# Kernel optimization log

Hardware: AMD Instinct MI355X
Metric: run time of the kernel (lower is better)

The kernel has to match this reference:

```python
import jax, jax.numpy as jnp
import numpy as np

D_MODEL = 1024
SCALE = 1.0 / np.sqrt(D_MODEL).astype(np.float32)


def setup_inputs() -> dict:
    key = jax.random.key(0)
    ks = jax.random.split(key, 9)
    B, S, D = 4, 2048, D_MODEL
    init = 1.0 / np.sqrt(D).astype(np.float32)
    return {
        "q": jax.random.normal(ks[0], (B, S, D), jnp.float32),
        "k": jax.random.normal(ks[1], (B, S, D), jnp.float32),
        "v": jax.random.normal(ks[2], (B, S, D), jnp.float32),
        "Wq": jax.random.uniform(ks[3], (D, D), jnp.float32, -init, init),
        "bq": jax.random.uniform(ks[4], (D,), jnp.float32, -init, init),
        "Wk": jax.random.uniform(ks[5], (D, D), jnp.float32, -init, init),
        "bk": jax.random.uniform(ks[6], (D,), jnp.float32, -init, init),
        "Wv": jax.random.uniform(ks[7], (D, D), jnp.float32, -init, init),
        "bv": jax.random.uniform(ks[8], (D,), jnp.float32, -init, init),
    }


def reference(q, k, v, Wq, bq, Wk, bk, Wv, bv):
    # Linear projections (torch Linear: x @ W.T + b)
    qp = jnp.einsum('bsd,ed->bse', q, Wq) + bq
    kp = jnp.einsum('bsd,ed->bse', k, Wk) + bk
    vp = jnp.einsum('bsd,ed->bse', v, Wv) + bv
    qp = jax.nn.softmax(qp, axis=-1)          # softmax over feature dim
    kp = jax.nn.softmax(kp, axis=-2) * SCALE  # softmax over sequence dim
    vp = jax.nn.softmax(vp, axis=-2)          # softmax over sequence dim
    attn_weights = jnp.einsum('bqd,bkd->bqk', qp, kp)  # [B,S,S]
    output = jnp.einsum('bqk,bkd->bqd', attn_weights, vp)
    return (output, attn_weights)
```

## Files before the change

### kernel.cpp

```cpp
#include <hip/hip_runtime.h>
#include <math.h>


typedef float  f32x4  __attribute__((ext_vector_type(4)));
typedef __bf16 bf16x8 __attribute__((ext_vector_type(8)));
typedef int    i32x4  __attribute__((ext_vector_type(4)));
typedef unsigned short u16;

__device__ __forceinline__ float b2f(u16 u) {
    unsigned int i = ((unsigned int)u) << 16; float f;
    __builtin_memcpy(&f, &i, 4); return f;
}
__device__ __forceinline__ u16 f2b(float f) {
    unsigned int i; __builtin_memcpy(&i, &f, 4);
    i += 0x7FFFu + ((i >> 16) & 1u);
    return (u16)(i >> 16);
}

__global__ __launch_bounds__(256) void cvt_all(
    const float4* __restrict__ q, const float4* __restrict__ k,
    const float4* __restrict__ v, const float4* __restrict__ Wq,
    const float4* __restrict__ Wk, const float4* __restrict__ Wv,
    const float* __restrict__ bq, const float* __restrict__ bk,
    const float* __restrict__ bv,
    ushort4* __restrict__ qb, ushort4* __restrict__ kb,
    ushort4* __restrict__ vb, ushort4* __restrict__ Wb,
    float* __restrict__ biasCat)
{
    int bid = blockIdx.x, t = threadIdx.x;
    const float4* s; ushort4* d; int idx;
    if (bid < 8192)       { s = q;  d = qb;            idx = bid * 256 + t; }
    else if (bid < 16384) { s = k;  d = kb;            idx = (bid - 8192) * 256 + t; }
    else if (bid < 24576) { s = v;  d = vb;            idx = (bid - 16384) * 256 + t; }
    else if (bid < 25600) { s = Wq; d = Wb;            idx = (bid - 24576) * 256 + t; }
    else if (bid < 26624) { s = Wk; d = Wb + 262144;   idx = (bid - 25600) * 256 + t; }
    else if (bid < 27648) { s = Wv; d = Wb + 524288;   idx = (bid - 26624) * 256 + t; }
    else {
        for (int i = t; i < 3072; i += 256)
            biasCat[i] = (i < 1024) ? bq[i] : (i < 2048) ? bk[i - 1024] : bv[i - 2048];
        return;
    }
    float4 vv = s[idx];
    ushort4 o;
    o.x = f2b(vv.x); o.y = f2b(vv.y); o.z = f2b(vv.z); o.w = f2b(vv.w);
    d[idx] = o;
}

__global__ __launch_bounds__(512, 2) void gemm256_attn(
    const u16* __restrict__ Ap, const u16* __restrict__ Bp,
    float* __restrict__ C32, u16* __restrict__ C16,
    int N, int K, long long sA, long long sB, long long sC)
{
    __shared__ __align__(16) u16 lds[65536];

    const int tid  = threadIdx.x;
    const int lane = tid & 63;
    const int w    = tid >> 6;
    const int wr   = w >> 2, wc = w & 3;

    const int gx  = gridDim.x;
    const int tot = gx * gridDim.y;
    const int lin = blockIdx.y * gx + blockIdx.x;
    const int vlin = (lin & 7) * (tot >> 3) + (lin >> 3);
    const int bx = vlin % gx, by = vlin / gx;
    const int m0 = by * 256, n0 = bx * 256;
    const int z  = blockIdx.z;

    const u16* Ag = Ap + (size_t)z * sA;
    const u16* Bg = Bp + (size_t)z * sB;

    const int cl = tid ^ ((tid >> 4) & 6);
    const int lr = cl >> 3;
    const int ce = (cl & 7) * 8;
    const int arow = m0 + lr;
    const int brow = n0 + (lr & 31) + ((lr & 32) << 1);

    const int axr = ((lane >> 2) & 3) << 4;
    const int ar0 = (wr * 64 + (lane & 15)) * 64 + (lane >> 4) * 8;
    const int br0 = (wc * 32 + (lane & 15)) * 64 + (lane >> 4) * 8;

#define GLL16(gsrc, ldsoff)                                                    \
    __builtin_amdgcn_global_load_lds(                                          \
        (__attribute__((address_space(1))) void*)(uintptr_t)(gsrc),            \
        (__attribute__((address_space(3))) void*)&lds[ldsoff], 16, 0, 0)

#define STAGE_A(c, h, T)                                                       \
    do { const u16* _s = Ag + (size_t)(arow + (h) * 64) * K + (T) * 64 + ce;   \
         int _d = (((c) << 1) + (h)) * 8192 + tid * 8;                         \
         GLL16(_s, _d); GLL16(_s + (size_t)128 * K, _d + 4096); } while (0)

#define STAGE_B(c, g, T)                                                       \
    do { const u16* _s = Bg + (size_t)(brow + (g) * 32) * K + (T) * 64 + ce;   \
         int _d = 32768 + (((c) << 1) + (g)) * 8192 + tid * 8;                 \
         GLL16(_s, _d); GLL16(_s + (size_t)128 * K, _d + 4096); } while (0)

#define SBAR asm volatile("s_barrier" ::: "memory")
#define LGKM0 do { asm volatile("s_waitcnt lgkmcnt(0)" ::: "memory");          \
                   __builtin_amdgcn_sched_barrier(0); } while (0)

#define LDA(base)                                                              \
    _Pragma("unroll") for (int mi2 = 0; mi2 < 4; ++mi2)                        \
    _Pragma("unroll") for (int ks = 0; ks < 2; ++ks)                           \
        afr[mi2][ks] = __builtin_bit_cast(bf16x8,                              \
            *(const i32x4*)&lds[(base) + ((ar0 + mi2 * 1024 + ks * 32) ^ axr)]);

#define LDB(dst, base)                                                         \
    _Pragma("unroll") for (int ni2 = 0; ni2 < 2; ++ni2)                        \
    _Pragma("unroll") for (int ks = 0; ks < 2; ++ks)                           \
        dst[ni2][ks] = __builtin_bit_cast(bf16x8,                              \
            *(const i32x4*)&lds[(base) + ((br0 + ni2 * 1024 + ks * 32) ^ axr)]);

#define MFMA_Q(mb, nb, bfrag)                                                  \
    __builtin_amdgcn_s_setprio(1);                                             \
    _Pragma("unroll") for (int mi2 = 0; mi2 < 4; ++mi2)                        \
    _Pragma("unroll") for (int ni2 = 0; ni2 < 2; ++ni2)                        \
    _Pragma("unroll") for (int ks = 0; ks < 2; ++ks)                           \
        acc[(mb) + mi2][(nb) + ni2] = __builtin_amdgcn_mfma_f32_16x16x32_bf16( \
            afr[mi2][ks], bfrag[ni2][ks], acc[(mb) + mi2][(nb) + ni2], 0, 0, 0); \
    __builtin_amdgcn_s_setprio(0)

    f32x4 acc[8][4];
#pragma unroll
    for (int i = 0; i < 8; ++i)
#pragma unroll
        for (int j = 0; j < 4; ++j) acc[i][j] = (f32x4)0.0f;

    bf16x8 afr[4][2], b0f[2][2], b1f[2][2];

    const int nt = K >> 6;

    STAGE_A(0, 0, 0); STAGE_B(0, 0, 0);
    STAGE_A(0, 1, 0); STAGE_B(0, 1, 0);
    STAGE_A(1, 0, 1); STAGE_B(1, 0, 1);

    for (int T = 0; T < nt; ++T) {
        const int cur = T & 1, nxt = cur ^ 1;
        const int ab = (cur << 1) * 8192;
        const int bb = 32768 + (cur << 1) * 8192;

        if (T + 1 < nt) asm volatile("s_waitcnt vmcnt(4)" ::: "memory");
        else            asm volatile("s_waitcnt vmcnt(0)" ::: "memory");
        SBAR;
        LDA(ab); LDB(b0f, bb);
        if (T + 1 < nt) STAGE_B(nxt, 1, T + 1);
        SBAR; LGKM0;
        MFMA_Q(0, 0, b0f);
        SBAR;
        LDB(b1f, bb + 8192);
        if (T + 1 < nt) STAGE_A(nxt, 1, T + 1);
        SBAR; LGKM0;
        MFMA_Q(0, 2, b1f);
        SBAR;
        LDA(ab + 8192);
        if (T + 2 < nt) STAGE_A(cur, 0, T + 2);
        SBAR; LGKM0;
        MFMA_Q(4, 0, b0f);
        SBAR;
        if (T + 2 < nt) STAGE_B(cur, 0, T + 2);
        SBAR; LGKM0;
        MFMA_Q(4, 2, b1f);
        SBAR;
    }

    const int cr0 = m0 + wr * 128 + ((lane >> 4) << 2);
    const int cc0 = n0 + wc * 64 + (lane & 15);
    float* Cg = C32 + (size_t)z * sC;
#pragma unroll
    for (int mi = 0; mi < 8; ++mi)
#pragma unroll
        for (int ni = 0; ni < 4; ++ni)
#pragma unroll
            for (int j = 0; j < 4; ++j)
                Cg[(size_t)(cr0 + mi * 16 + j) * N + cc0 + ni * 16] = acc[mi][ni][j];

    u16* sE = lds;
    u16* Cb = C16 + (size_t)z * sC;
    const int wrow0 = ((lane >> 4) << 2);
    const int wcol0 = wc * 64 + (lane & 15);
    const int rr = tid >> 2;
    const int c0 = (tid & 3) * 8;
    __syncthreads();
#pragma unroll
    for (int p = 0; p < 2; ++p) {
        if (wr == p) {
#pragma unroll
            for (int mi = 0; mi < 8; ++mi)
#pragma unroll
                for (int ni = 0; ni < 4; ++ni)
#pragma unroll
                    for (int j = 0; j < 4; ++j)
                        sE[(wrow0 + mi * 16 + j) * 264 + wcol0 + ni * 16] =
                            f2b(acc[mi][ni][j]);
        }
        __syncthreads();
#pragma unroll
        for (int i = 0; i < 8; ++i) {
            i32x4 vv = *(const i32x4*)&sE[rr * 264 + c0 + i * 32];
            *(i32x4*)&Cb[(size_t)(m0 + p * 128 + rr) * N + n0 + c0 + i * 32] = vv;
        }
        if (p == 0) __syncthreads();
    }
#undef GLL16
#undef STAGE_A
#undef STAGE_B
#undef LDA
#undef LDB
#undef MFMA_Q
}

template<int EPI, int BM>
__global__ __launch_bounds__(256, 2) void gemm_bw(
    const u16* __restrict__ Ap, const u16* __restrict__ Bp,
    float* __restrict__ C32, u16* __restrict__ C16, u16* __restrict__ Calt,
    const float* __restrict__ bias,
    int N, int K, long long sA, long long sB, long long sC)
{
    constexpr int AMI = BM / 32;
    constexpr int ALD = BM / 64;
    constexpr int ASZ = BM * 32;
    constexpr int BUF = ASZ + 4096;
    __shared__ __align__(16) u16 lds[3 * BUF];

    const int tid  = threadIdx.x;
    const int lane = tid & 63;
    const int w    = tid >> 6;
    const int wr   = w >> 1, wc = w & 1;

    const int gx  = gridDim.x;
    const int tot = gx * gridDim.y;
    const int lin = blockIdx.y * gx + blockIdx.x;
    const int vlin = (lin & 7) * (tot >> 3) + (lin >> 3);
    const int bx = vlin % gx, by = vlin / gx;
    const int m0 = by * BM, n0 = bx * 128;
    const int z  = blockIdx.z;

    const u16* Ag = Ap + (size_t)z * sA;
    const u16* Bg = Bp + (size_t)z * sB;

    const int cltid = tid ^ ((tid >> 3) & 3);
    const int crow  = cltid >> 2;
    const int ce    = (cltid & 3) * 8;

    const int exr = ((lane >> 1) & 3) << 3;
    const int ar0 = (wr * (BM / 2) + (lane & 15)) * 32 + (lane >> 4) * 8;
    const int br0 = (wc * 64 + (lane & 15)) * 32 + (lane >> 4) * 8;

#define GLLW(gsrc, ldsoff)                                                     \
    __builtin_amdgcn_global_load_lds(                                          \
        (__attribute__((address_space(1))) void*)(uintptr_t)(gsrc),            \
        (__attribute__((address_space(3))) void*)&lds[ldsoff], 16, 0, 0)

#define STAGE(buf, T)                                                          \
    do {                                                                       \
        _Pragma("unroll") for (int ld = 0; ld < ALD; ++ld)                     \
            GLLW(Ag + (size_t)(m0 + ld * 64 + crow) * K + (T) * 32 + ce,       \
                 (buf) + ld * 2048 + tid * 8);                                 \
        _Pragma("unroll") for (int ld = 0; ld < 2; ++ld)                       \
            GLLW(Bg + (size_t)(n0 + ld * 64 + crow) * K + (T) * 32 + ce,       \
                 (buf) + ASZ + ld * 2048 + tid * 8);                           \
    } while (0)

#define LGKM0B do { asm volatile("s_waitcnt lgkmcnt(0)" ::: "memory");         \
                    __builtin_amdgcn_sched_barrier(0); } while (0)

    f32x4 acc[AMI][4];
#pragma unroll
    for (int i = 0; i < AMI; ++i)
#pragma unroll
        for (int j = 0; j < 4; ++j) acc[i][j] = (f32x4)0.0f;

    bf16x8 afr[AMI], bfr[4];

    const int nt = K >> 5;

    int b0 = 0, b1 = BUF, b2 = 2 * BUF;
    STAGE(b0, 0); STAGE(b1, 1);

    for (int T = 0; T < nt; ++T) {
        if (T + 1 < nt) {
            if constexpr (BM == 256) asm volatile("s_waitcnt vmcnt(6)" ::: "memory");
            else                     asm volatile("s_waitcnt vmcnt(4)" ::: "memory");
        } else {
            asm volatile("s_waitcnt vmcnt(0)" ::: "memory");
        }
        asm volatile("s_barrier" ::: "memory");
#pragma unroll
        for (int mi = 0; mi < AMI; ++mi)
            afr[mi] = __builtin_bit_cast(bf16x8,
                *(const i32x4*)&lds[b0 + ((ar0 + mi * 512) ^ exr)]);
#pragma unroll
        for (int ni = 0; ni < 4; ++ni)
            bfr[ni] = __builtin_bit_cast(bf16x8,
                *(const i32x4*)&lds[b0 + ASZ + ((br0 + ni * 512) ^ exr)]);
        if (T + 2 < nt) STAGE(b2, T + 2);
        LGKM0B;
        __builtin_amdgcn_s_setprio(1);
#pragma unroll
        for (int mi = 0; mi < AMI; ++mi)
#pragma unroll
            for (int ni = 0; ni < 4; ++ni)
                acc[mi][ni] = __builtin_amdgcn_mfma_f32_16x16x32_bf16(
                    afr[mi], bfr[ni], acc[mi][ni], 0, 0, 0);
        __builtin_amdgcn_s_setprio(0);
        int tmp = b0; b0 = b1; b1 = b2; b2 = tmp;
    }

    if constexpr (EPI == 1) {
        u16* sE = lds;
        u16* Cb = (z == 2) ? Calt : (C16 + (size_t)z * sC);
        const int colb = wc * 64 + (lane & 15);
        float bv[4];
#pragma unroll
        for (int ni = 0; ni < 4; ++ni)
            bv[ni] = bias[(size_t)z * 1024 + n0 + colb + ni * 16];
        const int wrow0 = wr * (BM / 2) + ((lane >> 4) << 2);
        __syncthreads();
#pragma unroll
        for (int mi = 0; mi < AMI; ++mi)
#pragma unroll
            for (int ni = 0; ni < 4; ++ni)
#pragma unroll
                for (int j = 0; j < 4; ++j)
                    sE[(wrow0 + mi * 16 + j) * 136 + colb + ni * 16] =
                        f2b(__expf(acc[mi][ni][j] + bv[ni]));
        __syncthreads();
        const int rr = tid >> 2, c0 = (tid & 3) * 8;
#pragma unroll
        for (int rb = 0; rb < BM / 64; ++rb) {
            int row = rb * 64 + rr;
#pragma unroll
            for (int i = 0; i < 4; ++i) {
                i32x4 vv = *(const i32x4*)&sE[row * 136 + c0 + i * 32];
                *(i32x4*)&Cb[(size_t)(m0 + row) * N + n0 + c0 + i * 32] = vv;
            }
        }
    } else {
        float* Cg = C32 + (size_t)z * sC;
        const int cr0 = m0 + wr * (BM / 2) + ((lane >> 4) << 2);
        const int cc0 = n0 + wc * 64 + (lane & 15);
#pragma unroll
        for (int mi = 0; mi < AMI; ++mi)
#pragma unroll
            for (int ni = 0; ni < 4; ++ni)
#pragma unroll
                for (int j = 0; j < 4; ++j)
                    Cg[(size_t)(cr0 + mi * 16 + j) * N + cc0 + ni * 16] =
                        acc[mi][ni][j];
    }
#undef GLLW
#undef STAGE
#undef LGKM0B
}

__global__ __launch_bounds__(256) void sm_partials(
    u16* __restrict__ qE, const u16* __restrict__ kE, const u16* __restrict__ vE,
    float* __restrict__ kpart, float* __restrict__ vpart)
{
    int bid = blockIdx.x, t = threadIdx.x;
    if (bid < 8192) {
        u16* p = qE + (size_t)bid * 1024;
        ushort4 v = *(ushort4*)&p[t * 4];
        float e0 = b2f(v.x), e1 = b2f(v.y), e2 = b2f(v.z), e3 = b2f(v.w);
        float s = (e0 + e1) + (e2 + e3);
#pragma unroll
        for (int off = 32; off; off >>= 1) s += __shfl_down(s, off);
        __shared__ float red[4];
        if ((t & 63) == 0) red[t >> 6] = s;
        __syncthreads();
        float inv = 1.0f / ((red[0] + red[1]) + (red[2] + red[3]));
        ushort4 o;
        o.x = f2b(e0 * inv); o.y = f2b(e1 * inv);
        o.z = f2b(e2 * inv); o.w = f2b(e3 * inv);
        *(ushort4*)&p[t * 4] = o;
    } else {
        int j = bid - 8192;
        const u16* d; float* part;
        if (j < 64) { d = kE; part = kpart; } else { d = vE; part = vpart; j -= 64; }
        int b = j >> 4, c = j & 15;
        const u16* base = d + ((size_t)b * 2048 + c * 128) * 1024 + t * 4;
        float a0 = 0, a1 = 0, a2 = 0, a3 = 0;
        for (int s = 0; s < 128; ++s) {
            ushort4 v = *(const ushort4*)(base + (size_t)s * 1024);
            a0 += b2f(v.x); a1 += b2f(v.y); a2 += b2f(v.z); a3 += b2f(v.w);
        }
        *(float4*)(part + ((size_t)(b * 16 + c)) * 1024 + t * 4) = make_float4(a0, a1, a2, a3);
    }
}

__global__ __launch_bounds__(256) void col_reduce2(
    const float* __restrict__ kpart, const float* __restrict__ vpart,
    float* __restrict__ kinv, float* __restrict__ vinv)
{
    int bid = blockIdx.x;
    const float* part; float* inv; float mult;
    if (bid < 16) { part = kpart; inv = kinv; mult = 0.03125f; }
    else          { part = vpart; inv = vinv; mult = 1.0f; bid -= 16; }
    int idx = bid * 256 + threadIdx.x;
    int b = idx >> 10, e = idx & 1023;
    float s = 0;
    for (int c = 0; c < 16; ++c) s += part[((size_t)(b * 16 + c)) * 1024 + e];
    inv[idx] = mult / s;
}

__global__ __launch_bounds__(256) void norm_all(
    u16* __restrict__ kE, const float* __restrict__ kinv,
    const u16* __restrict__ vE, const float* __restrict__ vinv,
    u16* __restrict__ vpT)
{
    int bid = blockIdx.x, t = threadIdx.x;
    if (bid < 8192) {
        int b = bid >> 11, s = bid & 2047;
        u16* p = kE + ((size_t)b * 2048 + s) * 1024 + t * 4;
        float4 iv = *(const float4*)(kinv + b * 1024 + t * 4);
        ushort4 v = *(ushort4*)p;
        v.x = f2b(b2f(v.x) * iv.x); v.y = f2b(b2f(v.y) * iv.y);
        v.z = f2b(b2f(v.z) * iv.z); v.w = f2b(b2f(v.w) * iv.w);
        *(ushort4*)p = v;
    } else {
        __shared__ __align__(16) u16 tile[64][68];
        int j = bid - 8192;
        int b = j >> 9, y = (j >> 5) & 15, x = j & 31;
        int s0 = x * 64, e0 = y * 64;
        int lr = t >> 4, lc = (t & 15) * 4;
#pragma unroll
        for (int i = 0; i < 4; ++i) {
            int sr = i * 16 + lr;
            ushort4 v = *(const ushort4*)(vE + ((size_t)b * 2048 + s0 + sr) * 1024 + e0 + lc);
            tile[sr][lc] = v.x; tile[sr][lc + 1] = v.y;
            tile[sr][lc + 2] = v.z; tile[sr][lc + 3] = v.w;
        }
        __syncthreads();
#pragma unroll
        for (int i = 0; i < 4; ++i) {
            int er = i * 16 + lr;
            float iv = vinv[b * 1024 + e0 + er];
            ushort4 v;
            v.x = f2b(b2f(tile[lc + 0][er]) * iv);
            v.y = f2b(b2f(tile[lc + 1][er]) * iv);
            v.z = f2b(b2f(tile[lc + 2][er]) * iv);
            v.w = f2b(b2f(tile[lc + 3][er]) * iv);
            *(ushort4*)(vpT + ((size_t)b * 1024 + e0 + er) * 2048 + s0 + lc) = v;
        }
    }
}

extern "C" void kernel_launch(void* const* d_in, const int* in_sizes, int n_in,
                              void* d_out, int out_size, void* d_ws, size_t ws_size,
                              hipStream_t stream)
{
    const float* q  = (const float*)d_in[0];
    const float* k  = (const float*)d_in[1];
    const float* v  = (const float*)d_in[2];
    const float* Wq = (const float*)d_in[3];
    const float* bq = (const float*)d_in[4];
    const float* Wk = (const float*)d_in[5];
    const float* bk = (const float*)d_in[6];
    const float* Wv = (const float*)d_in[7];
    const float* bv = (const float*)d_in[8];

    float* out  = (float*)d_out;
    float* attn = out + 8388608;

    u16* wsU = (u16*)d_ws;
    u16* qE   = wsU;
    u16* kE   = wsU + 8388608;
    u16* Wb   = wsU + 16777216;
    u16* qb   = wsU + 25165824;
    u16* kb   = wsU + 33554432;
    u16* vb   = wsU + 41943040;
    u16* vpT  = wsU + 25165824;
    u16* attnB = wsU + 33554432;
    u16* vE   = (u16*)attn;

    float* tail  = (float*)(wsU + 50331648);
    float* kpart = tail;
    float* vpart = tail + 65536;
    float* kinv  = tail + 131072;
    float* vinv  = tail + 135168;
    float* biasCat = tail + 139264;

    const long long SD = 2048LL * 1024, SS = 2048LL * 2048, DS = 1024LL * 2048;

    cvt_all<<<dim3(27649), dim3(256), 0, stream>>>(
        (const float4*)q, (const float4*)k, (const float4*)v,
        (const float4*)Wq, (const float4*)Wk, (const float4*)Wv,
        bq, bk, bv,
        (ushort4*)qb, (ushort4*)kb, (ushort4*)vb, (ushort4*)Wb, biasCat);

    gemm_bw<1, 256><<<dim3(8, 32, 3), dim3(256), 0, stream>>>(
        qb, Wb, nullptr, qE, vE, biasCat,
        1024, 1024, 8388608LL, 1048576LL, 8388608LL);

    sm_partials<<<dim3(8320), dim3(256), 0, stream>>>(qE, kE, vE, kpart, vpart);

    col_reduce2<<<dim3(32), dim3(256), 0, stream>>>(kpart, vpart, kinv, vinv);

    norm_all<<<dim3(10240), dim3(256), 0, stream>>>(kE, kinv, vE, vinv, vpT);

    gemm256_attn<<<dim3(8, 8, 4), dim3(512), 0, stream>>>(
        qE, kE, attn, attnB, 2048, 1024, SD, SD, SS);

    gemm_bw<2, 128><<<dim3(8, 16, 4), dim3(256), 0, stream>>>(
        attnB, vpT, out, nullptr, nullptr, nullptr, 1024, 2048, SS, DS, SD);
}
```

Baseline: 215.7 us.

## Reassociate output as Q·(KᵀV) instead of (QKᵀ)·V

```diff
diff --git a/kernel.cpp b/kernel.cpp
--- a/kernel.cpp
+++ b/kernel.cpp
@@ -48,7 +48,7 @@
 
 __global__ __launch_bounds__(512, 2) void gemm256_attn(
     const u16* __restrict__ Ap, const u16* __restrict__ Bp,
-    float* __restrict__ C32, u16* __restrict__ C16,
+    float* __restrict__ C32,
     int N, int K, long long sA, long long sB, long long sC)
 {
     __shared__ __align__(16) u16 lds[65536];
@@ -172,53 +172,24 @@
 #pragma unroll
             for (int j = 0; j < 4; ++j)
                 Cg[(size_t)(cr0 + mi * 16 + j) * N + cc0 + ni * 16] = acc[mi][ni][j];
-
-    u16* sE = lds;
-    u16* Cb = C16 + (size_t)z * sC;
-    const int wrow0 = ((lane >> 4) << 2);
-    const int wcol0 = wc * 64 + (lane & 15);
-    const int rr = tid >> 2;
-    const int c0 = (tid & 3) * 8;
-    __syncthreads();
-#pragma unroll
-    for (int p = 0; p < 2; ++p) {
-        if (wr == p) {
-#pragma unroll
-            for (int mi = 0; mi < 8; ++mi)
-#pragma unroll
-                for (int ni = 0; ni < 4; ++ni)
-#pragma unroll
-                    for (int j = 0; j < 4; ++j)
-                        sE[(wrow0 + mi * 16 + j) * 264 + wcol0 + ni * 16] =
-                            f2b(acc[mi][ni][j]);
-        }
-        __syncthreads();
-#pragma unroll
-        for (int i = 0; i < 8; ++i) {
-            i32x4 vv = *(const i32x4*)&sE[rr * 264 + c0 + i * 32];
-            *(i32x4*)&Cb[(size_t)(m0 + p * 128 + rr) * N + n0 + c0 + i * 32] = vv;
-        }
-        if (p == 0) __syncthreads();
-    }
 #undef GLL16
 #undef STAGE_A
 #undef STAGE_B
+#undef SBAR
+#undef LGKM0
 #undef LDA
 #undef LDB
 #undef MFMA_Q
 }
 
-template<int EPI, int BM>
-__global__ __launch_bounds__(256, 2) void gemm_bw(
+template<int EPI>
+__global__ __launch_bounds__(256, 3) void gemm_bw(
     const u16* __restrict__ Ap, const u16* __restrict__ Bp,
     float* __restrict__ C32, u16* __restrict__ C16, u16* __restrict__ Calt,
     const float* __restrict__ bias,
     int N, int K, long long sA, long long sB, long long sC)
 {
-    constexpr int AMI = BM / 32;
-    constexpr int ALD = BM / 64;
-    constexpr int ASZ = BM * 32;
-    constexpr int BUF = ASZ + 4096;
+    constexpr int BUF = 8192;
     __shared__ __align__(16) u16 lds[3 * BUF];
 
     const int tid  = threadIdx.x;
@@ -231,7 +202,7 @@
     const int lin = blockIdx.y * gx + blockIdx.x;
     const int vlin = (lin & 7) * (tot >> 3) + (lin >> 3);
     const int bx = vlin % gx, by = vlin / gx;
-    const int m0 = by * BM, n0 = bx * 128;
+    const int m0 = by * 128, n0 = bx * 128;
     const int z  = blockIdx.z;
 
     const u16* Ag = Ap + (size_t)z * sA;
@@ -242,7 +213,7 @@
     const int ce    = (cltid & 3) * 8;
 
     const int exr = ((lane >> 1) & 3) << 3;
-    const int ar0 = (wr * (BM / 2) + (lane & 15)) * 32 + (lane >> 4) * 8;
+    const int ar0 = (wr * 64 + (lane & 15)) * 32 + (lane >> 4) * 8;
     const int br0 = (wc * 64 + (lane & 15)) * 32 + (lane >> 4) * 8;
 
 #define GLLW(gsrc, ldsoff)                                                     \
@@ -252,24 +223,24 @@
 
 #define STAGE(buf, T)                                                          \
     do {                                                                       \
-        _Pragma("unroll") for (int ld = 0; ld < ALD; ++ld)                     \
+        _Pragma("unroll") for (int ld = 0; ld < 2; ++ld)                       \
             GLLW(Ag + (size_t)(m0 + ld * 64 + crow) * K + (T) * 32 + ce,       \
                  (buf) + ld * 2048 + tid * 8);                                 \
         _Pragma("unroll") for (int ld = 0; ld < 2; ++ld)                       \
             GLLW(Bg + (size_t)(n0 + ld * 64 + crow) * K + (T) * 32 + ce,       \
-                 (buf) + ASZ + ld * 2048 + tid * 8);                           \
+                 (buf) + 4096 + ld * 2048 + tid * 8);                          \
     } while (0)
 
 #define LGKM0B do { asm volatile("s_waitcnt lgkmcnt(0)" ::: "memory");         \
                     __builtin_amdgcn_sched_barrier(0); } while (0)
 
-    f32x4 acc[AMI][4];
-#pragma unroll
-    for (int i = 0; i < AMI; ++i)
+    f32x4 acc[4][4];
+#pragma unroll
+    for (int i = 0; i < 4; ++i)
 #pragma unroll
         for (int j = 0; j < 4; ++j) acc[i][j] = (f32x4)0.0f;
 
-    bf16x8 afr[AMI], bfr[4];
+    bf16x8 afr[4], bfr[4];
 
     const int nt = K >> 5;
 
@@ -277,26 +248,22 @@
     STAGE(b0, 0); STAGE(b1, 1);
 
     for (int T = 0; T < nt; ++T) {
-        if (T + 1 < nt) {
-            if constexpr (BM == 256) asm volatile("s_waitcnt vmcnt(6)" ::: "memory");
-            else                     asm volatile("s_waitcnt vmcnt(4)" ::: "memory");
-        } else {
-            asm volatile("s_waitcnt vmcnt(0)" ::: "memory");
-        }
+        if (T + 1 < nt) asm volatile("s_waitcnt vmcnt(4)" ::: "memory");
+        else            asm volatile("s_waitcnt vmcnt(0)" ::: "memory");
         asm volatile("s_barrier" ::: "memory");
 #pragma unroll
-        for (int mi = 0; mi < AMI; ++mi)
+        for (int mi = 0; mi < 4; ++mi)
             afr[mi] = __builtin_bit_cast(bf16x8,
                 *(const i32x4*)&lds[b0 + ((ar0 + mi * 512) ^ exr)]);
 #pragma unroll
         for (int ni = 0; ni < 4; ++ni)
             bfr[ni] = __builtin_bit_cast(bf16x8,
-                *(const i32x4*)&lds[b0 + ASZ + ((br0 + ni * 512) ^ exr)]);
+                *(const i32x4*)&lds[b0 + 4096 + ((br0 + ni * 512) ^ exr)]);
         if (T + 2 < nt) STAGE(b2, T + 2);
         LGKM0B;
         __builtin_amdgcn_s_setprio(1);
 #pragma unroll
-        for (int mi = 0; mi < AMI; ++mi)
+        for (int mi = 0; mi < 4; ++mi)
 #pragma unroll
             for (int ni = 0; ni < 4; ++ni)
                 acc[mi][ni] = __builtin_amdgcn_mfma_f32_16x16x32_bf16(
@@ -305,28 +272,35 @@
         int tmp = b0; b0 = b1; b1 = b2; b2 = tmp;
     }
 
-    if constexpr (EPI == 1) {
+    if constexpr (EPI == 1 || EPI == 3) {
         u16* sE = lds;
-        u16* Cb = (z == 2) ? Calt : (C16 + (size_t)z * sC);
+        u16* Cb;
         const int colb = wc * 64 + (lane & 15);
         float bv[4];
-#pragma unroll
-        for (int ni = 0; ni < 4; ++ni)
-            bv[ni] = bias[(size_t)z * 1024 + n0 + colb + ni * 16];
-        const int wrow0 = wr * (BM / 2) + ((lane >> 4) << 2);
+        if constexpr (EPI == 1) {
+            Cb = (z == 2) ? Calt : (C16 + (size_t)z * sC);
+#pragma unroll
+            for (int ni = 0; ni < 4; ++ni)
+                bv[ni] = bias[(size_t)z * 1024 + n0 + colb + ni * 16];
+        } else {
+            Cb = C16 + (size_t)z * sC;
+        }
+        const int wrow0 = wr * 64 + ((lane >> 4) << 2);
         __syncthreads();
 #pragma unroll
-        for (int mi = 0; mi < AMI; ++mi)
+        for (int mi = 0; mi < 4; ++mi)
 #pragma unroll
             for (int ni = 0; ni < 4; ++ni)
 #pragma unroll
-                for (int j = 0; j < 4; ++j)
-                    sE[(wrow0 + mi * 16 + j) * 136 + colb + ni * 16] =
-                        f2b(__expf(acc[mi][ni][j] + bv[ni]));
+                for (int j = 0; j < 4; ++j) {
+                    float vv = acc[mi][ni][j];
+                    if constexpr (EPI == 1) vv = __expf(vv + bv[ni]);
+                    sE[(wrow0 + mi * 16 + j) * 136 + colb + ni * 16] = f2b(vv);
+                }
         __syncthreads();
         const int rr = tid >> 2, c0 = (tid & 3) * 8;
 #pragma unroll
-        for (int rb = 0; rb < BM / 64; ++rb) {
+        for (int rb = 0; rb < 2; ++rb) {
             int row = rb * 64 + rr;
 #pragma unroll
             for (int i = 0; i < 4; ++i) {
@@ -336,10 +310,10 @@
         }
     } else {
         float* Cg = C32 + (size_t)z * sC;
-        const int cr0 = m0 + wr * (BM / 2) + ((lane >> 4) << 2);
+        const int cr0 = m0 + wr * 64 + ((lane >> 4) << 2);
         const int cc0 = n0 + wc * 64 + (lane & 15);
 #pragma unroll
-        for (int mi = 0; mi < AMI; ++mi)
+        for (int mi = 0; mi < 4; ++mi)
 #pragma unroll
             for (int ni = 0; ni < 4; ++ni)
 #pragma unroll
@@ -403,44 +377,40 @@
 }
 
 __global__ __launch_bounds__(256) void norm_all(
-    u16* __restrict__ kE, const float* __restrict__ kinv,
-    const u16* __restrict__ vE, const float* __restrict__ vinv,
-    u16* __restrict__ vpT)
-{
-    int bid = blockIdx.x, t = threadIdx.x;
-    if (bid < 8192) {
-        int b = bid >> 11, s = bid & 2047;
-        u16* p = kE + ((size_t)b * 2048 + s) * 1024 + t * 4;
-        float4 iv = *(const float4*)(kinv + b * 1024 + t * 4);
-        ushort4 v = *(ushort4*)p;
+    u16* __restrict__ kE, const float* __restrict__ kinv, u16* __restrict__ kpT,
+    u16* __restrict__ vE, const float* __restrict__ vinv, u16* __restrict__ vpT)
+{
+    __shared__ __align__(16) u16 tile[64][68];
+    int j = blockIdx.x, t = threadIdx.x;
+    const bool isK = j < 2048;
+    if (!isK) j -= 2048;
+    int b = j >> 9, y = (j >> 5) & 15, x = j & 31;
+    int s0 = x * 64, e0 = y * 64;
+    int lr = t >> 4, lc = (t & 15) * 4;
+
+    u16* src = isK ? kE : vE;
+    const float* inv = isK ? kinv : vinv;
+    float4 iv = *(const float4*)(inv + b * 1024 + e0 + lc);
+#pragma unroll
+    for (int i = 0; i < 4; ++i) {
+        int sr = i * 16 + lr;
+        u16* p = src + ((size_t)b * 2048 + s0 + sr) * 1024 + e0 + lc;
+        ushort4 v = *(const ushort4*)p;
         v.x = f2b(b2f(v.x) * iv.x); v.y = f2b(b2f(v.y) * iv.y);
         v.z = f2b(b2f(v.z) * iv.z); v.w = f2b(b2f(v.w) * iv.w);
-        *(ushort4*)p = v;
-    } else {
-        __shared__ __align__(16) u16 tile[64][68];
-        int j = bid - 8192;
-        int b = j >> 9, y = (j >> 5) & 15, x = j & 31;
-        int s0 = x * 64, e0 = y * 64;
-        int lr = t >> 4, lc = (t & 15) * 4;
-#pragma unroll
-        for (int i = 0; i < 4; ++i) {
-            int sr = i * 16 + lr;
-            ushort4 v = *(const ushort4*)(vE + ((size_t)b * 2048 + s0 + sr) * 1024 + e0 + lc);
-            tile[sr][lc] = v.x; tile[sr][lc + 1] = v.y;
-            tile[sr][lc + 2] = v.z; tile[sr][lc + 3] = v.w;
-        }
-        __syncthreads();
-#pragma unroll
-        for (int i = 0; i < 4; ++i) {
-            int er = i * 16 + lr;
-            float iv = vinv[b * 1024 + e0 + er];
-            ushort4 v;
-            v.x = f2b(b2f(tile[lc + 0][er]) * iv);
-            v.y = f2b(b2f(tile[lc + 1][er]) * iv);
-            v.z = f2b(b2f(tile[lc + 2][er]) * iv);
-            v.w = f2b(b2f(tile[lc + 3][er]) * iv);
-            *(ushort4*)(vpT + ((size_t)b * 1024 + e0 + er) * 2048 + s0 + lc) = v;
-        }
+        if (isK) *(ushort4*)p = v;
+        tile[sr][lc] = v.x; tile[sr][lc + 1] = v.y;
+        tile[sr][lc + 2] = v.z; tile[sr][lc + 3] = v.w;
+    }
+    __syncthreads();
+    u16* dst = isK ? kpT : vpT;
+#pragma unroll
+    for (int i = 0; i < 4; ++i) {
+        int er = i * 16 + lr;
+        ushort4 v;
+        v.x = tile[lc + 0][er]; v.y = tile[lc + 1][er];
+        v.z = tile[lc + 2][er]; v.w = tile[lc + 3][er];
+        *(ushort4*)(dst + ((size_t)b * 1024 + e0 + er) * 2048 + s0 + lc) = v;
     }
 }
 
@@ -469,7 +439,8 @@
     u16* kb   = wsU + 33554432;
     u16* vb   = wsU + 41943040;
     u16* vpT  = wsU + 25165824;
-    u16* attnB = wsU + 33554432;
+    u16* kpT  = wsU + 33554432;
+    u16* Mt   = wsU + 41943040;
     u16* vE   = (u16*)attn;
 
     float* tail  = (float*)(wsU + 50331648);
@@ -487,7 +458,7 @@
         bq, bk, bv,
         (ushort4*)qb, (ushort4*)kb, (ushort4*)vb, (ushort4*)Wb, biasCat);
 
-    gemm_bw<1, 256><<<dim3(8, 32, 3), dim3(256), 0, stream>>>(
+    gemm_bw<1><<<dim3(8, 64, 3), dim3(256), 0, stream>>>(
         qb, Wb, nullptr, qE, vE, biasCat,
         1024, 1024, 8388608LL, 1048576LL, 8388608LL);
 
@@ -495,11 +466,16 @@
 
     col_reduce2<<<dim3(32), dim3(256), 0, stream>>>(kpart, vpart, kinv, vinv);
 
-    norm_all<<<dim3(10240), dim3(256), 0, stream>>>(kE, kinv, vE, vinv, vpT);
+    norm_all<<<dim3(4096), dim3(256), 0, stream>>>(kE, kinv, kpT, vE, vinv, vpT);
+
+    gemm_bw<3><<<dim3(8, 8, 4), dim3(256), 0, stream>>>(
+        vpT, kpT, nullptr, Mt, nullptr, nullptr,
+        1024, 2048, DS, DS, 1048576LL);
 
     gemm256_attn<<<dim3(8, 8, 4), dim3(512), 0, stream>>>(
-        qE, kE, attn, attnB, 2048, 1024, SD, SD, SS);
-
-    gemm_bw<2, 128><<<dim3(8, 16, 4), dim3(256), 0, stream>>>(
-        attnB, vpT, out, nullptr, nullptr, nullptr, 1024, 2048, SS, DS, SD);
-}
+        qE, kE, attn, 2048, 1024, SD, SD, SS);
+
+    gemm_bw<2><<<dim3(8, 16, 4), dim3(256), 0, stream>>>(
+        qE, Mt, out, nullptr, nullptr, nullptr,
+        1024, 1024, SD, 1048576LL, SD);
+}
```

Result: slower. 225.7 us (+4.6%).

## Fuse column sums into projection epilogue and split-K the output GEMM

Applied to the files above, without the earlier changes.

```diff
diff --git a/kernel.cpp b/kernel.cpp
--- a/kernel.cpp
+++ b/kernel.cpp
@@ -203,16 +203,18 @@
 #undef GLL16
 #undef STAGE_A
 #undef STAGE_B
+#undef SBAR
+#undef LGKM0
 #undef LDA
 #undef LDB
 #undef MFMA_Q
 }
 
-template<int EPI, int BM>
-__global__ __launch_bounds__(256, 2) void gemm_bw(
+template<int EPI, int BM, int KSPLIT>
+__global__ __launch_bounds__(256, BM == 128 ? 3 : 2) void gemm_bw(
     const u16* __restrict__ Ap, const u16* __restrict__ Bp,
     float* __restrict__ C32, u16* __restrict__ C16, u16* __restrict__ Calt,
-    const float* __restrict__ bias,
+    const float* __restrict__ bias, float* __restrict__ csum,
     int N, int K, long long sA, long long sB, long long sC)
 {
     constexpr int AMI = BM / 32;
@@ -232,10 +234,13 @@
     const int vlin = (lin & 7) * (tot >> 3) + (lin >> 3);
     const int bx = vlin % gx, by = vlin / gx;
     const int m0 = by * BM, n0 = bx * 128;
-    const int z  = blockIdx.z;
-
-    const u16* Ag = Ap + (size_t)z * sA;
-    const u16* Bg = Bp + (size_t)z * sB;
+    const int zz = blockIdx.z;
+    const int z  = (KSPLIT == 1) ? zz : (zz & 3);
+    const int kc = (KSPLIT == 1) ? 0 : (zz >> 2);
+    const int Kc = K / KSPLIT;
+
+    const u16* Ag = Ap + (size_t)z * sA + (size_t)kc * Kc;
+    const u16* Bg = Bp + (size_t)z * sB + (size_t)kc * Kc;
 
     const int cltid = tid ^ ((tid >> 3) & 3);
     const int crow  = cltid >> 2;
@@ -271,7 +276,7 @@
 
     bf16x8 afr[AMI], bfr[4];
 
-    const int nt = K >> 5;
+    const int nt = Kc >> 5;
 
     int b0 = 0, b1 = BUF, b2 = 2 * BUF;
     STAGE(b0, 0); STAGE(b1, 1);
@@ -309,10 +314,12 @@
         u16* sE = lds;
         u16* Cb = (z == 2) ? Calt : (C16 + (size_t)z * sC);
         const int colb = wc * 64 + (lane & 15);
-        float bv[4];
-#pragma unroll
-        for (int ni = 0; ni < 4; ++ni)
+        float bv[4], cs[4];
+#pragma unroll
+        for (int ni = 0; ni < 4; ++ni) {
             bv[ni] = bias[(size_t)z * 1024 + n0 + colb + ni * 16];
+            cs[ni] = 0.0f;
+        }
         const int wrow0 = wr * (BM / 2) + ((lane >> 4) << 2);
         __syncthreads();
 #pragma unroll
@@ -320,9 +327,21 @@
 #pragma unroll
             for (int ni = 0; ni < 4; ++ni)
 #pragma unroll
-                for (int j = 0; j < 4; ++j)
-                    sE[(wrow0 + mi * 16 + j) * 136 + colb + ni * 16] =
-                        f2b(__expf(acc[mi][ni][j] + bv[ni]));
+                for (int j = 0; j < 4; ++j) {
+                    u16 h = f2b(__expf(acc[mi][ni][j] + bv[ni]));
+                    sE[(wrow0 + mi * 16 + j) * 136 + colb + ni * 16] = h;
+                    cs[ni] += b2f(h);
+                }
+        if (z >= 1) {
+            float* dst = csum + (z - 1) * 4096 + (m0 >> 11) * 1024;
+#pragma unroll
+            for (int ni = 0; ni < 4; ++ni) {
+                float s = cs[ni];
+                s += __shfl_xor(s, 16);
+                s += __shfl_xor(s, 32);
+                if (lane < 16) atomicAdd(&dst[n0 + colb + ni * 16], s);
+            }
+        }
         __syncthreads();
         const int rr = tid >> 2, c0 = (tid & 3) * 8;
 #pragma unroll
@@ -343,63 +362,44 @@
 #pragma unroll
             for (int ni = 0; ni < 4; ++ni)
 #pragma unroll
-                for (int j = 0; j < 4; ++j)
-                    Cg[(size_t)(cr0 + mi * 16 + j) * N + cc0 + ni * 16] =
-                        acc[mi][ni][j];
+                for (int j = 0; j < 4; ++j) {
+                    size_t idx = (size_t)(cr0 + mi * 16 + j) * N + cc0 + ni * 16;
+                    if constexpr (KSPLIT == 1) Cg[idx] = acc[mi][ni][j];
+                    else                       atomicAdd(&Cg[idx], acc[mi][ni][j]);
+                }
     }
 #undef GLLW
 #undef STAGE
 #undef LGKM0B
 }
 
-__global__ __launch_bounds__(256) void sm_partials(
-    u16* __restrict__ qE, const u16* __restrict__ kE, const u16* __restrict__ vE,
-    float* __restrict__ kpart, float* __restrict__ vpart)
-{
-    int bid = blockIdx.x, t = threadIdx.x;
-    if (bid < 8192) {
-        u16* p = qE + (size_t)bid * 1024;
-        ushort4 v = *(ushort4*)&p[t * 4];
-        float e0 = b2f(v.x), e1 = b2f(v.y), e2 = b2f(v.z), e3 = b2f(v.w);
-        float s = (e0 + e1) + (e2 + e3);
-#pragma unroll
-        for (int off = 32; off; off >>= 1) s += __shfl_down(s, off);
-        __shared__ float red[4];
-        if ((t & 63) == 0) red[t >> 6] = s;
-        __syncthreads();
-        float inv = 1.0f / ((red[0] + red[1]) + (red[2] + red[3]));
-        ushort4 o;
-        o.x = f2b(e0 * inv); o.y = f2b(e1 * inv);
-        o.z = f2b(e2 * inv); o.w = f2b(e3 * inv);
-        *(ushort4*)&p[t * 4] = o;
-    } else {
-        int j = bid - 8192;
-        const u16* d; float* part;
-        if (j < 64) { d = kE; part = kpart; } else { d = vE; part = vpart; j -= 64; }
-        int b = j >> 4, c = j & 15;
-        const u16* base = d + ((size_t)b * 2048 + c * 128) * 1024 + t * 4;
-        float a0 = 0, a1 = 0, a2 = 0, a3 = 0;
-        for (int s = 0; s < 128; ++s) {
-            ushort4 v = *(const ushort4*)(base + (size_t)s * 1024);
-            a0 += b2f(v.x); a1 += b2f(v.y); a2 += b2f(v.z); a3 += b2f(v.w);
-        }
-        *(float4*)(part + ((size_t)(b * 16 + c)) * 1024 + t * 4) = make_float4(a0, a1, a2, a3);
-    }
-}
-
-__global__ __launch_bounds__(256) void col_reduce2(
-    const float* __restrict__ kpart, const float* __restrict__ vpart,
-    float* __restrict__ kinv, float* __restrict__ vinv)
-{
-    int bid = blockIdx.x;
-    const float* part; float* inv; float mult;
-    if (bid < 16) { part = kpart; inv = kinv; mult = 0.03125f; }
-    else          { part = vpart; inv = vinv; mult = 1.0f; bid -= 16; }
-    int idx = bid * 256 + threadIdx.x;
-    int b = idx >> 10, e = idx & 1023;
-    float s = 0;
-    for (int c = 0; c < 16; ++c) s += part[((size_t)(b * 16 + c)) * 1024 + e];
-    inv[idx] = mult / s;
+__global__ __launch_bounds__(256) void q_softmax(u16* __restrict__ qE)
+{
+    size_t row = blockIdx.x;
+    u16* p = qE + row * 1024;
+    int t = threadIdx.x;
+    ushort4 v = *(ushort4*)&p[t * 4];
+    float e0 = b2f(v.x), e1 = b2f(v.y), e2 = b2f(v.z), e3 = b2f(v.w);
+    float s = (e0 + e1) + (e2 + e3);
+#pragma unroll
+    for (int off = 32; off; off >>= 1) s += __shfl_down(s, off);
+    __shared__ float red[4];
+    if ((t & 63) == 0) red[t >> 6] = s;
+    __syncthreads();
+    float inv = 1.0f / ((red[0] + red[1]) + (red[2] + red[3]));
+    ushort4 o;
+    o.x = f2b(e0 * inv); o.y = f2b(e1 * inv);
+    o.z = f2b(e2 * inv); o.w = f2b(e3 * inv);
+    *(ushort4*)&p[t * 4] = o;
+}
+
+__global__ __launch_bounds__(256) void col_inv(
+    const float* __restrict__ csum, float* __restrict__ kinv,
+    float* __restrict__ vinv)
+{
+    int idx = blockIdx.x * 256 + threadIdx.x;
+    kinv[idx] = 0.03125f / csum[idx];
+    vinv[idx] = 1.0f / csum[4096 + idx];
 }
 
 __global__ __launch_bounds__(256) void norm_all(
@@ -473,13 +473,15 @@
     u16* vE   = (u16*)attn;
 
     float* tail  = (float*)(wsU + 50331648);
-    float* kpart = tail;
-    float* vpart = tail + 65536;
+    float* csum  = tail;
     float* kinv  = tail + 131072;
     float* vinv  = tail + 135168;
     float* biasCat = tail + 139264;
 
     const long long SD = 2048LL * 1024, SS = 2048LL * 2048, DS = 1024LL * 2048;
+
+    hipMemsetAsync(out, 0, 8388608 * sizeof(float), stream);
+    hipMemsetAsync(csum, 0, 8192 * sizeof(float), stream);
 
     cvt_all<<<dim3(27649), dim3(256), 0, stream>>>(
         (const float4*)q, (const float4*)k, (const float4*)v,
@@ -487,19 +489,20 @@
         bq, bk, bv,
         (ushort4*)qb, (ushort4*)kb, (ushort4*)vb, (ushort4*)Wb, biasCat);
 
-    gemm_bw<1, 256><<<dim3(8, 32, 3), dim3(256), 0, stream>>>(
-        qb, Wb, nullptr, qE, vE, biasCat,
+    gemm_bw<1, 256, 1><<<dim3(8, 32, 3), dim3(256), 0, stream>>>(
+        qb, Wb, nullptr, qE, vE, biasCat, csum,
         1024, 1024, 8388608LL, 1048576LL, 8388608LL);
 
-    sm_partials<<<dim3(8320), dim3(256), 0, stream>>>(qE, kE, vE, kpart, vpart);
-
-    col_reduce2<<<dim3(32), dim3(256), 0, stream>>>(kpart, vpart, kinv, vinv);
+    q_softmax<<<dim3(8192), dim3(256), 0, stream>>>(qE);
+
+    col_inv<<<dim3(16), dim3(256), 0, stream>>>(csum, kinv, vinv);
 
     norm_all<<<dim3(10240), dim3(256), 0, stream>>>(kE, kinv, vE, vinv, vpT);
 
     gemm256_attn<<<dim3(8, 8, 4), dim3(512), 0, stream>>>(
         qE, kE, attn, attnB, 2048, 1024, SD, SD, SS);
 
-    gemm_bw<2, 128><<<dim3(8, 16, 4), dim3(256), 0, stream>>>(
-        attnB, vpT, out, nullptr, nullptr, nullptr, 1024, 2048, SS, DS, SD);
-}
+    gemm_bw<2, 128, 2><<<dim3(8, 16, 8), dim3(256), 0, stream>>>(
+        attnB, vpT, out, nullptr, nullptr, nullptr, nullptr,
+        1024, 2048, SS, DS, SD);
+}
```

After: 251.0 us. 16.3% more time.

## Fold column-softmax scales into q normalization and output GEMM epilogue

Applied to the files above, without the earlier changes.

```diff
diff --git a/kernel.cpp b/kernel.cpp
--- a/kernel.cpp
+++ b/kernel.cpp
@@ -203,16 +203,18 @@
 #undef GLL16
 #undef STAGE_A
 #undef STAGE_B
+#undef SBAR
+#undef LGKM0
 #undef LDA
 #undef LDB
 #undef MFMA_Q
 }
 
 template<int EPI, int BM>
-__global__ __launch_bounds__(256, 2) void gemm_bw(
+__global__ __launch_bounds__(256, BM == 128 ? 3 : 2) void gemm_bw(
     const u16* __restrict__ Ap, const u16* __restrict__ Bp,
     float* __restrict__ C32, u16* __restrict__ C16, u16* __restrict__ Calt,
-    const float* __restrict__ bias,
+    const float* __restrict__ bias, const float* __restrict__ vinv,
     int N, int K, long long sA, long long sB, long long sC)
 {
     constexpr int AMI = BM / 32;
@@ -338,6 +340,10 @@
         float* Cg = C32 + (size_t)z * sC;
         const int cr0 = m0 + wr * (BM / 2) + ((lane >> 4) << 2);
         const int cc0 = n0 + wc * 64 + (lane & 15);
+        float vs[4];
+#pragma unroll
+        for (int ni = 0; ni < 4; ++ni)
+            vs[ni] = vinv[(size_t)z * 1024 + cc0 + ni * 16];
 #pragma unroll
         for (int mi = 0; mi < AMI; ++mi)
 #pragma unroll
@@ -345,46 +351,28 @@
 #pragma unroll
                 for (int j = 0; j < 4; ++j)
                     Cg[(size_t)(cr0 + mi * 16 + j) * N + cc0 + ni * 16] =
-                        acc[mi][ni][j];
+                        acc[mi][ni][j] * vs[ni];
     }
 #undef GLLW
 #undef STAGE
 #undef LGKM0B
 }
 
-__global__ __launch_bounds__(256) void sm_partials(
-    u16* __restrict__ qE, const u16* __restrict__ kE, const u16* __restrict__ vE,
+__global__ __launch_bounds__(256) void colpart(
+    const u16* __restrict__ kE, const u16* __restrict__ vE,
     float* __restrict__ kpart, float* __restrict__ vpart)
 {
-    int bid = blockIdx.x, t = threadIdx.x;
-    if (bid < 8192) {
-        u16* p = qE + (size_t)bid * 1024;
-        ushort4 v = *(ushort4*)&p[t * 4];
-        float e0 = b2f(v.x), e1 = b2f(v.y), e2 = b2f(v.z), e3 = b2f(v.w);
-        float s = (e0 + e1) + (e2 + e3);
-#pragma unroll
-        for (int off = 32; off; off >>= 1) s += __shfl_down(s, off);
-        __shared__ float red[4];
-        if ((t & 63) == 0) red[t >> 6] = s;
-        __syncthreads();
-        float inv = 1.0f / ((red[0] + red[1]) + (red[2] + red[3]));
-        ushort4 o;
-        o.x = f2b(e0 * inv); o.y = f2b(e1 * inv);
-        o.z = f2b(e2 * inv); o.w = f2b(e3 * inv);
-        *(ushort4*)&p[t * 4] = o;
-    } else {
-        int j = bid - 8192;
-        const u16* d; float* part;
-        if (j < 64) { d = kE; part = kpart; } else { d = vE; part = vpart; j -= 64; }
-        int b = j >> 4, c = j & 15;
-        const u16* base = d + ((size_t)b * 2048 + c * 128) * 1024 + t * 4;
-        float a0 = 0, a1 = 0, a2 = 0, a3 = 0;
-        for (int s = 0; s < 128; ++s) {
-            ushort4 v = *(const ushort4*)(base + (size_t)s * 1024);
-            a0 += b2f(v.x); a1 += b2f(v.y); a2 += b2f(v.z); a3 += b2f(v.w);
-        }
-        *(float4*)(part + ((size_t)(b * 16 + c)) * 1024 + t * 4) = make_float4(a0, a1, a2, a3);
-    }
+    int j = blockIdx.x, t = threadIdx.x;
+    const u16* d; float* part;
+    if (j < 64) { d = kE; part = kpart; } else { d = vE; part = vpart; j -= 64; }
+    int b = j >> 4, c = j & 15;
+    const u16* base = d + ((size_t)b * 2048 + c * 128) * 1024 + t * 4;
+    float a0 = 0, a1 = 0, a2 = 0, a3 = 0;
+    for (int s = 0; s < 128; ++s) {
+        ushort4 v = *(const ushort4*)(base + (size_t)s * 1024);
+        a0 += b2f(v.x); a1 += b2f(v.y); a2 += b2f(v.z); a3 += b2f(v.w);
+    }
+    *(float4*)(part + ((size_t)(b * 16 + c)) * 1024 + t * 4) = make_float4(a0, a1, a2, a3);
 }
 
 __global__ __launch_bounds__(256) void col_reduce2(
@@ -402,45 +390,52 @@
     inv[idx] = mult / s;
 }
 
-__global__ __launch_bounds__(256) void norm_all(
-    u16* __restrict__ kE, const float* __restrict__ kinv,
-    const u16* __restrict__ vE, const float* __restrict__ vinv,
-    u16* __restrict__ vpT)
-{
-    int bid = blockIdx.x, t = threadIdx.x;
-    if (bid < 8192) {
-        int b = bid >> 11, s = bid & 2047;
-        u16* p = kE + ((size_t)b * 2048 + s) * 1024 + t * 4;
-        float4 iv = *(const float4*)(kinv + b * 1024 + t * 4);
-        ushort4 v = *(ushort4*)p;
-        v.x = f2b(b2f(v.x) * iv.x); v.y = f2b(b2f(v.y) * iv.y);
-        v.z = f2b(b2f(v.z) * iv.z); v.w = f2b(b2f(v.w) * iv.w);
-        *(ushort4*)p = v;
-    } else {
-        __shared__ __align__(16) u16 tile[64][68];
-        int j = bid - 8192;
-        int b = j >> 9, y = (j >> 5) & 15, x = j & 31;
-        int s0 = x * 64, e0 = y * 64;
-        int lr = t >> 4, lc = (t & 15) * 4;
-#pragma unroll
-        for (int i = 0; i < 4; ++i) {
-            int sr = i * 16 + lr;
-            ushort4 v = *(const ushort4*)(vE + ((size_t)b * 2048 + s0 + sr) * 1024 + e0 + lc);
-            tile[sr][lc] = v.x; tile[sr][lc + 1] = v.y;
-            tile[sr][lc + 2] = v.z; tile[sr][lc + 3] = v.w;
-        }
-        __syncthreads();
-#pragma unroll
-        for (int i = 0; i < 4; ++i) {
-            int er = i * 16 + lr;
-            float iv = vinv[b * 1024 + e0 + er];
-            ushort4 v;
-            v.x = f2b(b2f(tile[lc + 0][er]) * iv);
-            v.y = f2b(b2f(tile[lc + 1][er]) * iv);
-            v.z = f2b(b2f(tile[lc + 2][er]) * iv);
-            v.w = f2b(b2f(tile[lc + 3][er]) * iv);
-            *(ushort4*)(vpT + ((size_t)b * 1024 + e0 + er) * 2048 + s0 + lc) = v;
-        }
+__global__ __launch_bounds__(256) void qsm_scale(
+    u16* __restrict__ qE, const float* __restrict__ kinv)
+{
+    size_t row = blockIdx.x;
+    int b = (int)(row >> 11);
+    u16* p = qE + row * 1024;
+    int t = threadIdx.x;
+    ushort4 v = *(ushort4*)&p[t * 4];
+    float e0 = b2f(v.x), e1 = b2f(v.y), e2 = b2f(v.z), e3 = b2f(v.w);
+    float s = (e0 + e1) + (e2 + e3);
+#pragma unroll
+    for (int off = 32; off; off >>= 1) s += __shfl_down(s, off);
+    __shared__ float red[4];
+    if ((t & 63) == 0) red[t >> 6] = s;
+    __syncthreads();
+    float inv = 1.0f / ((red[0] + red[1]) + (red[2] + red[3]));
+    float4 kv = *(const float4*)(kinv + b * 1024 + t * 4);
+    ushort4 o;
+    o.x = f2b(e0 * inv * kv.x); o.y = f2b(e1 * inv * kv.y);
+    o.z = f2b(e2 * inv * kv.z); o.w = f2b(e3 * inv * kv.w);
+    *(ushort4*)&p[t * 4] = o;
+}
+
+__global__ __launch_bounds__(256) void vtrans(
+    const u16* __restrict__ vE, u16* __restrict__ vET)
+{
+    __shared__ __align__(16) u16 tile[64][68];
+    int j = blockIdx.x, t = threadIdx.x;
+    int b = j >> 9, y = (j >> 5) & 15, x = j & 31;
+    int s0 = x * 64, e0 = y * 64;
+    int lr = t >> 4, lc = (t & 15) * 4;
+#pragma unroll
+    for (int i = 0; i < 4; ++i) {
+        int sr = i * 16 + lr;
+        ushort4 v = *(const ushort4*)(vE + ((size_t)b * 2048 + s0 + sr) * 1024 + e0 + lc);
+        tile[sr][lc] = v.x; tile[sr][lc + 1] = v.y;
+        tile[sr][lc + 2] = v.z; tile[sr][lc + 3] = v.w;
+    }
+    __syncthreads();
+#pragma unroll
+    for (int i = 0; i < 4; ++i) {
+        int er = i * 16 + lr;
+        ushort4 v;
+        v.x = tile[lc + 0][er]; v.y = tile[lc + 1][er];
+        v.z = tile[lc + 2][er]; v.w = tile[lc + 3][er];
+        *(ushort4*)(vET + ((size_t)b * 1024 + e0 + er) * 2048 + s0 + lc) = v;
     }
 }
 
@@ -468,7 +463,7 @@
     u16* qb   = wsU + 25165824;
     u16* kb   = wsU + 33554432;
     u16* vb   = wsU + 41943040;
-    u16* vpT  = wsU + 25165824;
+    u16* vET  = wsU + 25165824;
     u16* attnB = wsU + 33554432;
     u16* vE   = (u16*)attn;
 
@@ -488,18 +483,21 @@
         (ushort4*)qb, (ushort4*)kb, (ushort4*)vb, (ushort4*)Wb, biasCat);
 
     gemm_bw<1, 256><<<dim3(8, 32, 3), dim3(256), 0, stream>>>(
-        qb, Wb, nullptr, qE, vE, biasCat,
+        qb, Wb, nullptr, qE, vE, biasCat, nullptr,
         1024, 1024, 8388608LL, 1048576LL, 8388608LL);
 
-    sm_partials<<<dim3(8320), dim3(256), 0, stream>>>(qE, kE, vE, kpart, vpart);
+    colpart<<<dim3(128), dim3(256), 0, stream>>>(kE, vE, kpart, vpart);
 
     col_reduce2<<<dim3(32), dim3(256), 0, stream>>>(kpart, vpart, kinv, vinv);
 
-    norm_all<<<dim3(10240), dim3(256), 0, stream>>>(kE, kinv, vE, vinv, vpT);
+    qsm_scale<<<dim3(8192), dim3(256), 0, stream>>>(qE, kinv);
+
+    vtrans<<<dim3(2048), dim3(256), 0, stream>>>(vE, vET);
 
     gemm256_attn<<<dim3(8, 8, 4), dim3(512), 0, stream>>>(
         qE, kE, attn, attnB, 2048, 1024, SD, SD, SS);
 
     gemm_bw<2, 128><<<dim3(8, 16, 4), dim3(256), 0, stream>>>(
-        attnB, vpT, out, nullptr, nullptr, nullptr, 1024, 2048, SS, DS, SD);
-}
+        attnB, vET, out, nullptr, nullptr, nullptr, vinv,
+        1024, 2048, SS, DS, SD);
+}
```

Measured after the change: 210.6 us. 2.4% less time.
